# Optimization experiments

Measured on AMD Instinct MI355X. Metric: run time of the kernel, lower is better.

## Reference

```python
import jax, jax.numpy as jnp
import numpy as np

N = 50000          # num graph nodes
E = 800000         # edges per direction
NGRAM, ODIM = 4, 32
DIMS = [128, 128, 64]
CLASSES = 128
MAXPE = 10
L2_EPS = 1e-12


def setup_inputs() -> dict:
    key = jax.random.key(0)
    ks = iter(jax.random.split(key, 40))
    d = {}
    d['x'] = jax.random.normal(next(ks), (N, DIMS[0]), jnp.float32)
    d['edge_index_in'] = jax.random.randint(next(ks), (2, E), 0, N, dtype=jnp.int64)
    d['edge_weight_in'] = jax.random.uniform(next(ks), (E,), jnp.float32)
    d['edge_index_out'] = jax.random.randint(next(ks), (2, E), 0, N, dtype=jnp.int64)
    d['edge_weight_out'] = jax.random.uniform(next(ks), (E,), jnp.float32)
    d['pe_table'] = jax.random.normal(next(ks), (MAXPE, ODIM), jnp.float32) * 0.05
    # per-layer DirectGCNLayer params (weights stored [in,out], i.e. torch W.T)
    for l in range(2):
        di, do = DIMS[l], DIMS[l + 1]
        s = 1.0 / np.sqrt(di)
        d[f'W_main_in_{l}'] = jax.random.normal(next(ks), (di, do), jnp.float32) * s
        d[f'W_main_out_{l}'] = jax.random.normal(next(ks), (di, do), jnp.float32) * s
        d[f'W_shared_{l}'] = jax.random.normal(next(ks), (di, do), jnp.float32) * s
        d[f'b_main_in_{l}'] = jnp.zeros((do,), jnp.float32)
        d[f'b_main_out_{l}'] = jnp.zeros((do,), jnp.float32)
        d[f'b_shared_in_{l}'] = jnp.zeros((do,), jnp.float32)
        d[f'b_shared_out_{l}'] = jnp.zeros((do,), jnp.float32)
        d[f'C_in_{l}'] = jnp.ones((N, 1), jnp.float32)
        d[f'C_out_{l}'] = jnp.ones((N, 1), jnp.float32)
    # residual projection for layer 1 (128 -> 64); layer 0 is identity
    d['res_W_1'] = jax.random.normal(next(ks), (DIMS[1], DIMS[2]), jnp.float32) * (1.0 / np.sqrt(DIMS[1]))
    d['res_b_1'] = jnp.zeros((DIMS[2],), jnp.float32)
    d['dec_W'] = jax.random.normal(next(ks), (DIMS[2], CLASSES), jnp.float32) * (1.0 / np.sqrt(DIMS[2]))
    d['dec_b'] = jnp.zeros((CLASSES,), jnp.float32)
    return d


def _prop(xW, ei, ew):
    # gather source, scale by edge weight, scatter-add to target (PyG aggr='add')
    return jax.ops.segment_sum(ew[:, None] * xW[ei[0]], ei[1], num_segments=N)


def _layer(h, ei_in, ew_in, ei_out, ew_out,
           Wmi, Wmo, Ws, bmi, bmo, bsi, bso, cin, cout):
    xs = h @ Ws  # shared transform, propagated over both edge sets
    ic = _prop(h @ Wmi, ei_in, ew_in) + bmi + _prop(xs, ei_in, ew_in) + bsi
    oc = _prop(h @ Wmo, ei_out, ew_out) + bmo + _prop(xs, ei_out, ew_out) + bso
    return cin * ic + cout * oc


def reference(x, edge_index_in, edge_weight_in, edge_index_out, edge_weight_out,
              pe_table,
              W_main_in_0, W_main_out_0, W_shared_0, b_main_in_0, b_main_out_0,
              b_shared_in_0, b_shared_out_0, C_in_0, C_out_0,
              W_main_in_1, W_main_out_1, W_shared_1, b_main_in_1, b_main_out_1,
              b_shared_in_1, b_shared_out_1, C_in_1, C_out_1,
              res_W_1, res_b_1, dec_W, dec_b):
    # positional encoding: add pe[:n_gram_len] to each n-gram slot
    h = (x.reshape(N, NGRAM, ODIM) + pe_table[:NGRAM][None]).reshape(N, NGRAM * ODIM)
    # layer 0 (identity residual); dropout p=0 / eval -> no-op
    h = jnp.tanh(_layer(h, edge_index_in, edge_weight_in, edge_index_out, edge_weight_out,
                        W_main_in_0, W_main_out_0, W_shared_0, b_main_in_0, b_main_out_0,
                        b_shared_in_0, b_shared_out_0, C_in_0, C_out_0) + h)
    # layer 1 (linear residual projection 128 -> 64)
    h = jnp.tanh(_layer(h, edge_index_in, edge_weight_in, edge_index_out, edge_weight_out,
                        W_main_in_1, W_main_out_1, W_shared_1, b_main_in_1, b_main_out_1,
                        b_shared_in_1, b_shared_out_1, C_in_1, C_out_1)
                 + h @ res_W_1 + res_b_1)
    logits = h @ dec_W + dec_b
    logp = jax.nn.log_softmax(logits, axis=-1)
    emb = h / (jnp.linalg.norm(h, axis=1, keepdims=True) + L2_EPS)
    return logp, emb
```

## Files before the change

### kernel.cpp

```cpp
#include <hip/hip_runtime.h>
#include <hip/hip_bf16.h>
#include <math.h>

typedef __hip_bfloat16  bf16;
typedef __hip_bfloat162 bf162;
typedef __attribute__((ext_vector_type(8))) short short8;
typedef __attribute__((ext_vector_type(4))) float floatx4;
typedef __attribute__((ext_vector_type(2))) float floatx2;

#define BSZ     128
#define NBMAX   512
#define PACHUNK 8192

__device__ inline float4 bf4_to_f4(uint2 v) {
  float2 lo = __bfloat1622float2(*(bf162*)&v.x);
  float2 hi = __bfloat1622float2(*(bf162*)&v.y);
  return make_float4(lo.x, lo.y, hi.x, hi.y);
}
__device__ inline uint2 f4_to_bf4(float4 v) {
  bf162 lo = __float22bfloat162_rn(make_float2(v.x, v.y));
  bf162 hi = __float22bfloat162_rn(make_float2(v.z, v.w));
  uint2 r;
  r.x = *(unsigned*)&lo;
  r.y = *(unsigned*)&hi;
  return r;
}
__device__ inline floatx2 bf2_to_f2(unsigned u) {
  floatx2 r;
  r.x = __uint_as_float(u << 16);
  r.y = __uint_as_float(u & 0xffff0000u);
  return r;
}

__global__ __launch_bounds__(256) void k_bhist(const int* __restrict__ eiIn, const int* __restrict__ eiOut,
                                               int E, int* __restrict__ bcnt, int NB) {
  __shared__ int h[NBMAX];
  const int t = threadIdx.x;
  const int set = blockIdx.y;
  const int* dst = (set ? eiOut : eiIn) + E;
  for (int i = t; i < NB; i += 256) h[i] = 0;
  __syncthreads();
  const int base = blockIdx.x * PACHUNK;
  const int m = min(PACHUNK, E - base);
  #pragma unroll 4
  for (int r = 0; r < PACHUNK / 256; ++r) {
    int i = r * 256 + t;
    if (i < m) atomicAdd(&h[dst[base + i] >> 7], 1);
  }
  __syncthreads();
  for (int i = t; i < NB; i += 256) {
    int c = h[i];
    if (c) atomicAdd(&bcnt[set * NBMAX + i], c);
  }
}

__global__ __launch_bounds__(64) void k_bscan(const int* __restrict__ bcnt,
                                              int* __restrict__ BO, int* __restrict__ bcur, int NB) {
  const int set = blockIdx.x;
  const int t = threadIdx.x;
  int carry = 0;
  for (int base = 0; base < NB; base += 64) {
    int idx = base + t;
    int v = (idx < NB) ? bcnt[set * NBMAX + idx] : 0;
    int incl = v;
    #pragma unroll
    for (int d = 1; d < 64; d <<= 1) {
      int u = __shfl_up(incl, d, 64);
      if (t >= d) incl += u;
    }
    if (idx < NB) {
      int e = carry + incl - v;
      BO[set * NBMAX + idx]   = e;
      bcur[set * NBMAX + idx] = e;
    }
    carry += __shfl(incl, 63, 64);
  }
}

__global__ __launch_bounds__(256) void k_partA(const int* __restrict__ eiIn, const float* __restrict__ ewIn,
                                               const int* __restrict__ eiOut, const float* __restrict__ ewOut,
                                               int E, int* __restrict__ bucketCur,
                                               int2* __restrict__ sI, int2* __restrict__ sO, int NB) {
  __shared__ int2 staged[PACHUNK];
  __shared__ int cnt[NBMAX];
  __shared__ int sb[NBMAX];
  const int t = threadIdx.x;
  const int set = blockIdx.y;
  const int*   ei = set ? eiOut : eiIn;
  const float* ew = set ? ewOut : ewIn;
  int2* stg  = set ? sO : sI;
  int*  bcur = bucketCur + set * NBMAX;
  const int base = blockIdx.x * PACHUNK;
  const int m = min(PACHUNK, E - base);
  for (int b = t; b < NB; b += 256) cnt[b] = 0;
  __syncthreads();
  #pragma unroll 4
  for (int r = 0; r < PACHUNK / 256; ++r) {
    int i = r * 256 + t;
    if (i < m) atomicAdd(&cnt[ei[E + base + i] >> 7], 1);
  }
  __syncthreads();
  if (t < 64) {
    int carry = 0;
    int nch = (NB + 63) >> 6;
    for (int c = 0; c < nch; ++c) {
      int idx = c * 64 + t;
      int v = (idx < NB) ? cnt[idx] : 0;
      int incl = v;
      #pragma unroll
      for (int d = 1; d < 64; d <<= 1) {
        int u = __shfl_up(incl, d, 64);
        if (t >= d) incl += u;
      }
      if (idx < NB) sb[idx] = carry + incl - v;
      carry += __shfl(incl, 63, 64);
    }
  }
  __syncthreads();
  for (int b = t; b < NB; b += 256) {
    int c = cnt[b];
    if (c > 0) cnt[b] = atomicAdd(&bcur[b], c) - sb[b];
  }
  __syncthreads();
  #pragma unroll 4
  for (int r = 0; r < PACHUNK / 256; ++r) {
    int i = r * 256 + t;
    if (i < m) {
      int src = ei[base + i];
      int dst = ei[E + base + i];
      float w = ew[base + i];
      int b = dst >> 7;
      int rank = atomicAdd(&sb[b], 1);
      staged[rank] = make_int2(src | ((dst & 127) << 16) | (b << 23), __float_as_int(w));
    }
  }
  __syncthreads();
  #pragma unroll 4
  for (int r = 0; r < PACHUNK / 256; ++r) {
    int j = r * 256 + t;
    if (j < m) {
      int2 p = staged[j];
      int b = ((unsigned)p.x) >> 23;
      stg[cnt[b] + j] = p;
    }
  }
}

__global__ __launch_bounds__(256) void k_partB(const int* __restrict__ BO, const int* __restrict__ bcur,
                                               const int2* __restrict__ sI, const int2* __restrict__ sO,
                                               int2* __restrict__ eI, int2* __restrict__ eO,
                                               int* __restrict__ offsI, int* __restrict__ offsO, int N) {
  __shared__ int cnt[BSZ];
  __shared__ int excl[BSZ];
  __shared__ int cur[BSZ];
  const int t = threadIdx.x;
  const int b = blockIdx.x;
  const int set = blockIdx.y;
  const int2* stg = set ? sO : sI;
  int2* out = set ? eO : eI;
  int*  offs = set ? offsO : offsI;
  const int nlo = b << 7;
  const int nodes = min(BSZ, N - nlo);
  const int lo = BO[set * NBMAX + b];
  const int hi = bcur[set * NBMAX + b];
  if (t < BSZ) cnt[t] = 0;
  __syncthreads();
  for (int i = lo + t; i < hi; i += 256) atomicAdd(&cnt[(stg[i].x >> 16) & 127], 1);
  __syncthreads();
  if (t < 64) {
    int v0 = cnt[t];
    int i0 = v0;
    #pragma unroll
    for (int d = 1; d < 64; d <<= 1) { int u = __shfl_up(i0, d, 64); if (t >= d) i0 += u; }
    int v1 = cnt[64 + t];
    int i1 = v1;
    #pragma unroll
    for (int d = 1; d < 64; d <<= 1) { int u = __shfl_up(i1, d, 64); if (t >= d) i1 += u; }
    int tot0 = __shfl(i0, 63, 64);
    excl[t]      = i0 - v0;
    excl[64 + t] = tot0 + i1 - v1;
  }
  __syncthreads();
  if (t < BSZ) cur[t] = lo + excl[t];
  if (t < nodes) offs[nlo + t] = lo + excl[t];
  if (b == gridDim.x - 1 && t == 0) offs[N] = hi;
  __syncthreads();
  for (int i = lo + t; i < hi; i += 256) {
    int2 p = stg[i];
    int dl = (p.x >> 16) & 127;
    int pos = atomicAdd(&cur[dl], 1);
    out[pos] = make_int2(p.x & 0xffff, p.y);
  }
}

__device__ inline void pack_one(const float* __restrict__ W, bf16* __restrict__ P,
                                int id, int NT, int DO) {
  int lane = id & 63;
  int tile = id >> 6;
  int nt = tile % NT, kt = tile / NT;
  int col  = nt * 16 + (lane & 15);
  int krow = kt * 32 + (lane >> 4) * 8;
  bf16* dst = P + (size_t)id * 8;
  #pragma unroll
  for (int j = 0; j < 8; ++j) dst[j] = __float2bfloat16(W[(size_t)(krow + j) * DO + col]);
}
__global__ void k_packall(const float* __restrict__ Wmi0, const float* __restrict__ Wmo0,
                          const float* __restrict__ Ws0,
                          const float* __restrict__ Wmi1, const float* __restrict__ Wmo1,
                          const float* __restrict__ Ws1,
                          const float* __restrict__ resW, const float* __restrict__ Wd,
                          const float* __restrict__ bmi0, const float* __restrict__ bsi0,
                          const float* __restrict__ bmo0, const float* __restrict__ bso0,
                          const float* __restrict__ bmi1, const float* __restrict__ bsi1,
                          const float* __restrict__ bmo1, const float* __restrict__ bso1,
                          bf16* __restrict__ P0, bf16* __restrict__ P1, bf16* __restrict__ Pd,
                          float* __restrict__ bi0, float* __restrict__ bo0,
                          float* __restrict__ bi1, float* __restrict__ bo1) {
  int id = blockIdx.x * blockDim.x + threadIdx.x;
  const int T0 = 8 * 8 * 64;
  const int T1 = 4 * 12 * 64;
  const int Td = 2 * 8 * 64;
  if (id < T0) {
    int lane = id & 63, tile = id >> 6;
    int nt = tile % 8, kt = tile / 8;
    int col  = nt * 16 + (lane & 15);
    int krow = kt * 32 + (lane >> 4) * 8;
    bf16* dst = P0 + (size_t)id * 8;
    #pragma unroll
    for (int j = 0; j < 8; ++j) {
      int r = krow + j;
      float v = (r < 128 ? Wmi0[r * 128 + col] : Wmo0[(r - 128) * 128 + col])
              + Ws0[(r & 127) * 128 + col];
      dst[j] = __float2bfloat16(v);
    }
  } else if (id < T0 + T1) {
    int id1 = id - T0;
    int lane = id1 & 63, tile = id1 >> 6;
    int nt = tile % 12, kt = tile / 12;
    int col  = nt * 16 + (lane & 15);
    int krow = kt * 32 + (lane >> 4) * 8;
    bf16* dst = P1 + (size_t)id1 * 8;
    #pragma unroll
    for (int j = 0; j < 8; ++j) {
      int kp = krow + j;
      int k = ((kp & 7) << 4) + (kp >> 3);
      float v;
      if (col < 64)       v = Wmi1[k * 64 + col]       + Ws1[k * 64 + col];
      else if (col < 128) v = Wmo1[k * 64 + col - 64]  + Ws1[k * 64 + col - 64];
      else                v = resW[k * 64 + col - 128];
      dst[j] = __float2bfloat16(v);
    }
  } else if (id < T0 + T1 + Td) {
    pack_one(Wd, Pd, id - T0 - T1, 8, 128);
  } else {
    int j = id - (T0 + T1 + Td);
    if (j < 128) { bi0[j] = bmi0[j] + bsi0[j]; bo0[j] = bmo0[j] + bso0[j]; }
    if (j < 64)  { bi1[j] = bmi1[j] + bsi1[j]; bo1[j] = bmo1[j] + bso1[j]; }
  }
}

__global__ void k_prep0(const float* __restrict__ x, const float* __restrict__ pe,
                        bf16* __restrict__ h0, int total) {
  int i = blockIdx.x * blockDim.x + threadIdx.x;
  if (i < total) h0[i] = __float2bfloat16(x[i] + pe[i & 127]);
}

__global__ __launch_bounds__(256) void k_agg0(const bf16* __restrict__ tb,
                                              const int* __restrict__ offsI, const int2* __restrict__ eI,
                                              const int* __restrict__ offsO, const int2* __restrict__ eO,
                                              const float* __restrict__ cin, const float* __restrict__ cou,
                                              bf16* __restrict__ aggC, int N) {
  int n = (blockIdx.x * blockDim.x + threadIdx.x) >> 6;
  int lane = threadIdx.x & 63;
  if (n >= N) return;
  const int dir = lane >> 5;
  const int sub = (lane >> 4) & 1;
  const int sl  = lane & 15;
  const int*   offs = dir ? offsO : offsI;
  const int2*  el   = dir ? eO : eI;
  const float* cc   = dir ? cou : cin;
  const char* base = (const char*)tb + sl * 16;
  floatx2 A0 = {0.f, 0.f}, A1 = {0.f, 0.f}, A2 = {0.f, 0.f}, A3 = {0.f, 0.f};
  const int s0 = offs[n], s1 = offs[n + 1];
  int i = s0 + sub;
  for (; i + 6 < s1; i += 8) {
    int2 eA = el[i], eB = el[i + 2], eC = el[i + 4], eD = el[i + 6];
    uint4 vA = *(const uint4*)(base + ((size_t)(unsigned)eA.x << 8));
    uint4 vB = *(const uint4*)(base + ((size_t)(unsigned)eB.x << 8));
    uint4 vC = *(const uint4*)(base + ((size_t)(unsigned)eC.x << 8));
    uint4 vD = *(const uint4*)(base + ((size_t)(unsigned)eD.x << 8));
    float fA = __int_as_float(eA.y), fB = __int_as_float(eB.y);
    float fC = __int_as_float(eC.y), fD = __int_as_float(eD.y);
    floatx2 wA = {fA, fA}, wB = {fB, fB}, wC = {fC, fC}, wD = {fD, fD};
    A0 += wA * bf2_to_f2(vA.x) + wB * bf2_to_f2(vB.x) + wC * bf2_to_f2(vC.x) + wD * bf2_to_f2(vD.x);
    A1 += wA * bf2_to_f2(vA.y) + wB * bf2_to_f2(vB.y) + wC * bf2_to_f2(vC.y) + wD * bf2_to_f2(vD.y);
    A2 += wA * bf2_to_f2(vA.z) + wB * bf2_to_f2(vB.z) + wC * bf2_to_f2(vC.z) + wD * bf2_to_f2(vD.z);
    A3 += wA * bf2_to_f2(vA.w) + wB * bf2_to_f2(vB.w) + wC * bf2_to_f2(vC.w) + wD * bf2_to_f2(vD.w);
  }
  for (; i < s1; i += 2) {
    int2 e = el[i];
    uint4 v = *(const uint4*)(base + ((size_t)(unsigned)e.x << 8));
    float f = __int_as_float(e.y);
    floatx2 w2 = {f, f};
    A0 += w2 * bf2_to_f2(v.x);
    A1 += w2 * bf2_to_f2(v.y);
    A2 += w2 * bf2_to_f2(v.z);
    A3 += w2 * bf2_to_f2(v.w);
  }
  float a0 = A0.x, a1 = A0.y, a2 = A1.x, a3 = A1.y;
  float a4 = A2.x, a5 = A2.y, a6 = A3.x, a7 = A3.y;
  a0 += __shfl_xor(a0, 16, 64); a1 += __shfl_xor(a1, 16, 64);
  a2 += __shfl_xor(a2, 16, 64); a3 += __shfl_xor(a3, 16, 64);
  a4 += __shfl_xor(a4, 16, 64); a5 += __shfl_xor(a5, 16, 64);
  a6 += __shfl_xor(a6, 16, 64); a7 += __shfl_xor(a7, 16, 64);
  if (sub == 0) {
    float c = cc[n];
    uint2 plo = f4_to_bf4(make_float4(c * a0, c * a1, c * a2, c * a3));
    uint2 phi = f4_to_bf4(make_float4(c * a4, c * a5, c * a6, c * a7));
    *(uint4*)(aggC + (size_t)n * 256 + dir * 128 + sl * 8) = make_uint4(plo.x, plo.y, phi.x, phi.y);
  }
}

__global__ __launch_bounds__(256) void k_mf01(const bf16* __restrict__ A,
                                              const bf16* __restrict__ Wp0,
                                              const bf16* __restrict__ Wp1,
                                              const float* __restrict__ bi, const float* __restrict__ bo,
                                              const float* __restrict__ cin, const float* __restrict__ cou,
                                              const bf16* __restrict__ h0,
                                              bf16* __restrict__ t1g, bf16* __restrict__ t1r, int N) {
  __shared__ bf16 hs[64][136];
  const int lane = threadIdx.x & 63;
  const int wid  = threadIdx.x >> 6;
  const int quad = lane >> 4, lc = lane & 15;
  const int bmw = blockIdx.x * 64 + wid * 16;
  const int rowc = min(bmw + lc, N - 1);
  const bf16* ap = A + (size_t)rowc * 256 + quad * 8;
  const short8* bp = (const short8*)Wp0 + lane;
  floatx4 acc[8] = {};
  #pragma unroll
  for (int kt = 0; kt < 8; ++kt) {
    short8 af = *(const short8*)(ap + kt * 32);
    #pragma unroll
    for (int nt = 0; nt < 8; ++nt) {
      short8 bfr = bp[(kt * 8 + nt) * 64];
      acc[nt] = __builtin_amdgcn_mfma_f32_16x16x32_bf16(af, bfr, acc[nt], 0, 0, 0);
    }
  }
  float bif[8], bof[8];
  #pragma unroll
  for (int nt = 0; nt < 8; ++nt) {
    bif[nt] = bi[nt * 16 + lc];
    bof[nt] = bo[nt * 16 + lc];
  }
  #pragma unroll
  for (int r = 0; r < 4; ++r) {
    int gmc = min(bmw + quad * 4 + r, N - 1);
    float ci = cin[gmc], co = cou[gmc];
    unsigned hp[4];
    #pragma unroll
    for (int np = 0; np < 4; ++np) {
      int n0 = 2 * np, n1 = 2 * np + 1;
      float v0 = acc[n0][r] + ci * bif[n0] + co * bof[n0]
               + __bfloat162float(h0[(size_t)gmc * 128 + n0 * 16 + lc]);
      float v1 = acc[n1][r] + ci * bif[n1] + co * bof[n1]
               + __bfloat162float(h0[(size_t)gmc * 128 + n1 * 16 + lc]);
      bf162 p = __float22bfloat162_rn(make_float2(tanhf(v0), tanhf(v1)));
      hp[np] = *(unsigned*)&p;
    }
    *(uint4*)(&hs[wid * 16 + quad * 4 + r][lc * 8]) = make_uint4(hp[0], hp[1], hp[2], hp[3]);
  }
  __syncthreads();
  const short8* bp1 = (const short8*)Wp1 + lane;
  floatx4 acc2[12] = {};
  #pragma unroll
  for (int kt = 0; kt < 4; ++kt) {
    short8 af = *(const short8*)(&hs[wid * 16 + lc][kt * 32 + quad * 8]);
    #pragma unroll
    for (int nt = 0; nt < 12; ++nt) {
      short8 bfr = bp1[(kt * 12 + nt) * 64];
      acc2[nt] = __builtin_amdgcn_mfma_f32_16x16x32_bf16(af, bfr, acc2[nt], 0, 0, 0);
    }
  }
  #pragma unroll
  for (int r = 0; r < 4; ++r) {
    int gm = bmw + quad * 4 + r;
    if (gm < N) {
      #pragma unroll
      for (int nt = 0; nt < 12; ++nt) {
        int col = nt * 16 + lc;
        bf16 v = __float2bfloat16(acc2[nt][r]);
        if (col < 128) t1g[(size_t)gm * 128 + col]        = v;
        else           t1r[(size_t)gm * 64 + (col - 128)] = v;
      }
    }
  }
}

__global__ __launch_bounds__(256) void k_agg1(const bf16* __restrict__ t1g, const bf16* __restrict__ t1r,
                                              const int* __restrict__ offsI, const int2* __restrict__ eI,
                                              const int* __restrict__ offsO, const int2* __restrict__ eO,
                                              const float* __restrict__ bi, const float* __restrict__ bo,
                                              const float* __restrict__ resb,
                                              const float* __restrict__ cin, const float* __restrict__ cou,
                                              bf16* __restrict__ h2b, float* __restrict__ emb, int N) {
  int n = (blockIdx.x * blockDim.x + threadIdx.x) >> 6;
  int lane = threadIdx.x & 63;
  if (n >= N) return;
  const int dir = lane >> 5;
  const int sub = (lane >> 3) & 3;
  const int sl  = lane & 7;
  const int*   offs = dir ? offsO : offsI;
  const int2*  el   = dir ? eO : eI;
  const char* base = (const char*)t1g + dir * 128 + sl * 16;
  floatx2 A0 = {0.f, 0.f}, A1 = {0.f, 0.f}, A2 = {0.f, 0.f}, A3 = {0.f, 0.f};
  const int s0 = offs[n], s1 = offs[n + 1];
  int i = s0 + sub;
  for (; i + 12 < s1; i += 16) {
    int2 eA = el[i], eB = el[i + 4], eC = el[i + 8], eD = el[i + 12];
    uint4 vA = *(const uint4*)(base + ((size_t)(unsigned)eA.x << 8));
    uint4 vB = *(const uint4*)(base + ((size_t)(unsigned)eB.x << 8));
    uint4 vC = *(const uint4*)(base + ((size_t)(unsigned)eC.x << 8));
    uint4 vD = *(const uint4*)(base + ((size_t)(unsigned)eD.x << 8));
    float fA = __int_as_float(eA.y), fB = __int_as_float(eB.y);
    float fC = __int_as_float(eC.y), fD = __int_as_float(eD.y);
    floatx2 wA = {fA, fA}, wB = {fB, fB}, wC = {fC, fC}, wD = {fD, fD};
    A0 += wA * bf2_to_f2(vA.x) + wB * bf2_to_f2(vB.x) + wC * bf2_to_f2(vC.x) + wD * bf2_to_f2(vD.x);
    A1 += wA * bf2_to_f2(vA.y) + wB * bf2_to_f2(vB.y) + wC * bf2_to_f2(vC.y) + wD * bf2_to_f2(vD.y);
    A2 += wA * bf2_to_f2(vA.z) + wB * bf2_to_f2(vB.z) + wC * bf2_to_f2(vC.z) + wD * bf2_to_f2(vD.z);
    A3 += wA * bf2_to_f2(vA.w) + wB * bf2_to_f2(vB.w) + wC * bf2_to_f2(vC.w) + wD * bf2_to_f2(vD.w);
  }
  for (; i < s1; i += 4) {
    int2 e = el[i];
    uint4 v = *(const uint4*)(base + ((size_t)(unsigned)e.x << 8));
    float f = __int_as_float(e.y);
    floatx2 w2 = {f, f};
    A0 += w2 * bf2_to_f2(v.x);
    A1 += w2 * bf2_to_f2(v.y);
    A2 += w2 * bf2_to_f2(v.z);
    A3 += w2 * bf2_to_f2(v.w);
  }
  float a0 = A0.x, a1 = A0.y, a2 = A1.x, a3 = A1.y;
  float a4 = A2.x, a5 = A2.y, a6 = A3.x, a7 = A3.y;
  a0 += __shfl_xor(a0, 8, 64);  a1 += __shfl_xor(a1, 8, 64);
  a2 += __shfl_xor(a2, 8, 64);  a3 += __shfl_xor(a3, 8, 64);
  a4 += __shfl_xor(a4, 8, 64);  a5 += __shfl_xor(a5, 8, 64);
  a6 += __shfl_xor(a6, 8, 64);  a7 += __shfl_xor(a7, 8, 64);
  a0 += __shfl_xor(a0, 16, 64); a1 += __shfl_xor(a1, 16, 64);
  a2 += __shfl_xor(a2, 16, 64); a3 += __shfl_xor(a3, 16, 64);
  a4 += __shfl_xor(a4, 16, 64); a5 += __shfl_xor(a5, 16, 64);
  a6 += __shfl_xor(a6, 16, 64); a7 += __shfl_xor(a7, 16, 64);
  float b0 = __shfl_xor(a0, 32, 64), b1 = __shfl_xor(a1, 32, 64);
  float b2 = __shfl_xor(a2, 32, 64), b3 = __shfl_xor(a3, 32, 64);
  float b4 = __shfl_xor(a4, 32, 64), b5 = __shfl_xor(a5, 32, 64);
  float b6 = __shfl_xor(a6, 32, 64), b7 = __shfl_xor(a7, 32, 64);
  if (sub == 0) {
    const int c = sl * 8;
    float ci = cin[n], co = cou[n];
    float s_in[8]  = { dir ? b0 : a0, dir ? b1 : a1, dir ? b2 : a2, dir ? b3 : a3,
                       dir ? b4 : a4, dir ? b5 : a5, dir ? b6 : a6, dir ? b7 : a7 };
    float s_ou[8]  = { dir ? a0 : b0, dir ? a1 : b1, dir ? a2 : b2, dir ? a3 : b3,
                       dir ? a4 : b4, dir ? a5 : b5, dir ? a6 : b6, dir ? a7 : b7 };
    float4 bif0 = *(const float4*)(bi + c),   bif1 = *(const float4*)(bi + c + 4);
    float4 bof0 = *(const float4*)(bo + c),   bof1 = *(const float4*)(bo + c + 4);
    float4 rbf0 = *(const float4*)(resb + c), rbf1 = *(const float4*)(resb + c + 4);
    uint4 rvu = *(const uint4*)((const char*)t1r + (size_t)n * 128 + sl * 16);
    float4 rv0 = bf4_to_f4(make_uint2(rvu.x, rvu.y));
    float4 rv1 = bf4_to_f4(make_uint2(rvu.z, rvu.w));
    float bif[8] = { bif0.x, bif0.y, bif0.z, bif0.w, bif1.x, bif1.y, bif1.z, bif1.w };
    float bof[8] = { bof0.x, bof0.y, bof0.z, bof0.w, bof1.x, bof1.y, bof1.z, bof1.w };
    float rbf[8] = { rbf0.x, rbf0.y, rbf0.z, rbf0.w, rbf1.x, rbf1.y, rbf1.z, rbf1.w };
    float rvf[8] = { rv0.x, rv0.y, rv0.z, rv0.w, rv1.x, rv1.y, rv1.z, rv1.w };
    float v[8];
    float q = 0.f;
    #pragma unroll
    for (int k = 0; k < 8; ++k) {
      v[k] = tanhf(ci * (s_in[k] + bif[k]) + co * (s_ou[k] + bof[k]) + rvf[k] + rbf[k]);
      q += v[k] * v[k];
    }
    q += __shfl_xor(q, 1, 64);
    q += __shfl_xor(q, 2, 64);
    q += __shfl_xor(q, 4, 64);
    if (dir == 0) {
      uint2 plo = f4_to_bf4(make_float4(v[0], v[1], v[2], v[3]));
      uint2 phi = f4_to_bf4(make_float4(v[4], v[5], v[6], v[7]));
      *(uint4*)(h2b + (size_t)n * 64 + c) = make_uint4(plo.x, plo.y, phi.x, phi.y);
    } else {
      float inv = 1.0f / (sqrtf(q) + 1e-12f);
      *(float4*)(emb + (size_t)n * 64 + c)     = make_float4(v[0] * inv, v[1] * inv, v[2] * inv, v[3] * inv);
      *(float4*)(emb + (size_t)n * 64 + c + 4) = make_float4(v[4] * inv, v[5] * inv, v[6] * inv, v[7] * inv);
    }
  }
}

__global__ __launch_bounds__(256) void k_mfd(const bf16* __restrict__ A,
                                             const bf16* __restrict__ Wp,
                                             const float* __restrict__ bd,
                                             float* __restrict__ logp, int N) {
  const int lane = threadIdx.x & 63;
  const int quad = lane >> 4, lc = lane & 15;
  const int bmw = blockIdx.x * 64 + (threadIdx.x >> 6) * 16;
  const int rowc = min(bmw + lc, N - 1);
  const bf16* ap = A + (size_t)rowc * 64 + quad * 8;
  const short8* bp = (const short8*)Wp + lane;
  floatx4 acc[8] = {};
  #pragma unroll
  for (int kt = 0; kt < 2; ++kt) {
    short8 af = *(const short8*)(ap + kt * 32);
    #pragma unroll
    for (int nt = 0; nt < 8; ++nt) {
      short8 bfr = bp[(kt * 8 + nt) * 64];
      acc[nt] = __builtin_amdgcn_mfma_f32_16x16x32_bf16(af, bfr, acc[nt], 0, 0, 0);
    }
  }
  float bdv[8];
  #pragma unroll
  for (int nt = 0; nt < 8; ++nt) bdv[nt] = bd[nt * 16 + lc];
  #pragma unroll
  for (int r = 0; r < 4; ++r) {
    int gm = bmw + quad * 4 + r;
    float v[8];
    #pragma unroll
    for (int nt = 0; nt < 8; ++nt) v[nt] = acc[nt][r] + bdv[nt];
    float m = v[0];
    #pragma unroll
    for (int nt = 1; nt < 8; ++nt) m = fmaxf(m, v[nt]);
    #pragma unroll
    for (int d = 1; d < 16; d <<= 1) m = fmaxf(m, __shfl_xor(m, d, 64));
    float s = 0.f;
    #pragma unroll
    for (int nt = 0; nt < 8; ++nt) s += __expf(v[nt] - m);
    #pragma unroll
    for (int d = 1; d < 16; d <<= 1) s += __shfl_xor(s, d, 64);
    float lse = m + __logf(s);
    if (gm < N) {
      #pragma unroll
      for (int nt = 0; nt < 8; ++nt) logp[(size_t)gm * 128 + nt * 16 + lc] = v[nt] - lse;
    }
  }
}

extern "C" void kernel_launch(void* const* d_in, const int* in_sizes, int n_in,
                              void* d_out, int out_size, void* d_ws, size_t ws_size,
                              hipStream_t stream) {
  const float* x     = (const float*)d_in[0];
  const int*   ei_in = (const int*)d_in[1];
  const float* ew_in = (const float*)d_in[2];
  const int*   ei_ou = (const int*)d_in[3];
  const float* ew_ou = (const float*)d_in[4];
  const float* pe    = (const float*)d_in[5];
  const float* Wmi0  = (const float*)d_in[6];
  const float* Wmo0  = (const float*)d_in[7];
  const float* Wsh0  = (const float*)d_in[8];
  const float* bmi0  = (const float*)d_in[9];
  const float* bmo0  = (const float*)d_in[10];
  const float* bsi0  = (const float*)d_in[11];
  const float* bso0  = (const float*)d_in[12];
  const float* cin0  = (const float*)d_in[13];
  const float* cou0  = (const float*)d_in[14];
  const float* Wmi1  = (const float*)d_in[15];
  const float* Wmo1  = (const float*)d_in[16];
  const float* Wsh1  = (const float*)d_in[17];
  const float* bmi1  = (const float*)d_in[18];
  const float* bmo1  = (const float*)d_in[19];
  const float* bsi1  = (const float*)d_in[20];
  const float* bso1  = (const float*)d_in[21];
  const float* cin1  = (const float*)d_in[22];
  const float* cou1  = (const float*)d_in[23];
  const float* resW  = (const float*)d_in[24];
  const float* resb  = (const float*)d_in[25];
  const float* Wd    = (const float*)d_in[26];
  const float* bd    = (const float*)d_in[27];

  const int N = in_sizes[0] / 128;
  const int E = in_sizes[2];
  const int NB = (N + BSZ - 1) >> 7;

  char* ws = (char*)d_ws;
  size_t off = 0;
  auto alloc = [&](size_t bytes) -> char* {
    off = (off + 255) & ~(size_t)255;
    char* p = ws + off;
    off += bytes;
    return p;
  };
  bf16*  h0bf  = (bf16*)alloc((size_t)N * 128 * 2);
  bf16*  aggC  = (bf16*)alloc((size_t)N * 256 * 2);
  bf16*  h2b   = (bf16*)alloc((size_t)N * 64 * 2);
  bf16*  Wp0   = (bf16*)alloc(256 * 128 * 2);
  bf16*  Wp1   = (bf16*)alloc(128 * 192 * 2);
  bf16*  Wpd   = (bf16*)alloc(64 * 128 * 2);
  float* bi0   = (float*)alloc(128 * 4);
  float* bo0   = (float*)alloc(128 * 4);
  float* bi1   = (float*)alloc(64 * 4);
  float* bo1   = (float*)alloc(64 * 4);
  int*   bcnt  = (int*)alloc((size_t)2 * NBMAX * 4);
  int*   BO    = (int*)alloc((size_t)2 * NBMAX * 4);
  int*   bcur  = (int*)alloc((size_t)2 * NBMAX * 4);
  int*   offsI = (int*)alloc((size_t)(N + 1) * 4);
  int*   offsO = (int*)alloc((size_t)(N + 1) * 4);
  int2*  sI    = (int2*)alloc((size_t)E * 8);
  int2*  sO    = (int2*)alloc((size_t)E * 8);
  int2*  eI    = (int2*)alloc((size_t)E * 8);
  int2*  eO    = (int2*)alloc((size_t)E * 8);
  bf16* t1g = aggC;
  bf16* t1r = t1g + (size_t)N * 128;

  (void)hipMemsetAsync(bcnt, 0, (size_t)2 * NBMAX * 4, stream);

  dim3 gc((E + PACHUNK - 1) / PACHUNK, 2);
  k_bhist<<<gc, 256, 0, stream>>>(ei_in, ei_ou, E, bcnt, NB);
  k_bscan<<<2, 64, 0, stream>>>(bcnt, BO, bcur, NB);
  k_partA<<<gc, 256, 0, stream>>>(ei_in, ew_in, ei_ou, ew_ou, E, bcur, sI, sO, NB);
  dim3 gb(NB, 2);
  k_partB<<<gb, 256, 0, stream>>>(BO, bcur, sI, sO, eI, eO, offsI, offsO, N);
  k_packall<<<(8 * 8 * 64 + 4 * 12 * 64 + 2 * 8 * 64 + 128 + 255) / 256, 256, 0, stream>>>(
      Wmi0, Wmo0, Wsh0, Wmi1, Wmo1, Wsh1, resW, Wd,
      bmi0, bsi0, bmo0, bso0, bmi1, bsi1, bmo1, bso1,
      Wp0, Wp1, Wpd, bi0, bo0, bi1, bo1);
  k_prep0<<<(N * 128 + 255) / 256, 256, 0, stream>>>(x, pe, h0bf, N * 128);

  int ab = (N + 3) / 4;
  int mb = (N + 63) / 64;
  k_agg0<<<ab, 256, 0, stream>>>(h0bf, offsI, eI, offsO, eO, cin0, cou0, aggC, N);
  k_mf01<<<mb, 256, 0, stream>>>(aggC, Wp0, Wp1, bi0, bo0, cin0, cou0, h0bf, t1g, t1r, N);

  float* logp = (float*)d_out;
  float* emb  = logp + (size_t)N * 128;
  k_agg1<<<ab, 256, 0, stream>>>(t1g, t1r, offsI, eI, offsO, eO, bi1, bo1, resb, cin1, cou1,
                                 h2b, emb, N);
  k_mfd<<<mb, 256, 0, stream>>>(h2b, Wpd, bd, logp, N);
}
```

Baseline: 350.3 us.

## Slice layer-0 features into per-XCD column slabs for L2-local gathers

The bf16 input features are stored as four 32-column slabs, one per slice, instead of row-major. The layer-0 aggregation grid is remapped so that each slice is handled by blocks on a fixed pair of XCDs. The intent is that each XCD's L2 only caches a quarter of the feature table during the random gather. The kernel now launches 4x more blocks, and each one gathers 64-byte row fragments with 4 edges in flight per lane group. The residual read in k_mf01 is updated to the sliced layout, and the partition chunk size is halved.

```diff
diff --git a/kernel.cpp b/kernel.cpp
--- a/kernel.cpp
+++ b/kernel.cpp
@@ -10,7 +10,7 @@
 
 #define BSZ     128
 #define NBMAX   512
-#define PACHUNK 8192
+#define PACHUNK 4096
 
 __device__ inline float4 bf4_to_f4(uint2 v) {
   float2 lo = __bfloat1622float2(*(bf162*)&v.x);
@@ -260,64 +260,70 @@
 }
 
 __global__ void k_prep0(const float* __restrict__ x, const float* __restrict__ pe,
-                        bf16* __restrict__ h0, int total) {
+                        bf16* __restrict__ h0s, int N) {
   int i = blockIdx.x * blockDim.x + threadIdx.x;
-  if (i < total) h0[i] = __float2bfloat16(x[i] + pe[i & 127]);
-}
-
-__global__ __launch_bounds__(256) void k_agg0(const bf16* __restrict__ tb,
+  if (i >= N * 128) return;
+  int c = i & 31;
+  int t = i >> 5;
+  int s = t / N;
+  int n = t - s * N;
+  int d = s * 32 + c;
+  h0s[i] = __float2bfloat16(x[(size_t)n * 128 + d] + pe[d]);
+}
+
+__global__ __launch_bounds__(256) void k_agg0(const bf16* __restrict__ tbS,
                                               const int* __restrict__ offsI, const int2* __restrict__ eI,
                                               const int* __restrict__ offsO, const int2* __restrict__ eO,
                                               const float* __restrict__ cin, const float* __restrict__ cou,
                                               bf16* __restrict__ aggC, int N) {
-  int n = (blockIdx.x * blockDim.x + threadIdx.x) >> 6;
-  int lane = threadIdx.x & 63;
+  const int b = blockIdx.x;
+  const int xcd = b & 7;
+  const int slice = xcd >> 1;
+  const int half = xcd & 1;
+  const int worker = (b >> 3) * 2 + half;
+  const int wid = threadIdx.x >> 6;
+  const int lane = threadIdx.x & 63;
+  const int n = worker * 4 + wid;
   if (n >= N) return;
   const int dir = lane >> 5;
-  const int sub = (lane >> 4) & 1;
-  const int sl  = lane & 15;
+  const int sub = (lane >> 3) & 3;
+  const int sl  = lane & 7;
   const int*   offs = dir ? offsO : offsI;
   const int2*  el   = dir ? eO : eI;
   const float* cc   = dir ? cou : cin;
-  const char* base = (const char*)tb + sl * 16;
-  floatx2 A0 = {0.f, 0.f}, A1 = {0.f, 0.f}, A2 = {0.f, 0.f}, A3 = {0.f, 0.f};
+  const char* base = (const char*)tbS + (size_t)slice * N * 64 + sl * 8;
+  floatx2 A0 = {0.f, 0.f}, A1 = {0.f, 0.f};
   const int s0 = offs[n], s1 = offs[n + 1];
   int i = s0 + sub;
-  for (; i + 6 < s1; i += 8) {
-    int2 eA = el[i], eB = el[i + 2], eC = el[i + 4], eD = el[i + 6];
-    uint4 vA = *(const uint4*)(base + ((size_t)(unsigned)eA.x << 8));
-    uint4 vB = *(const uint4*)(base + ((size_t)(unsigned)eB.x << 8));
-    uint4 vC = *(const uint4*)(base + ((size_t)(unsigned)eC.x << 8));
-    uint4 vD = *(const uint4*)(base + ((size_t)(unsigned)eD.x << 8));
+  for (; i + 12 < s1; i += 16) {
+    int2 eA = el[i], eB = el[i + 4], eC = el[i + 8], eD = el[i + 12];
+    uint2 vA = *(const uint2*)(base + ((size_t)(unsigned)eA.x << 6));
+    uint2 vB = *(const uint2*)(base + ((size_t)(unsigned)eB.x << 6));
+    uint2 vC = *(const uint2*)(base + ((size_t)(unsigned)eC.x << 6));
+    uint2 vD = *(const uint2*)(base + ((size_t)(unsigned)eD.x << 6));
     float fA = __int_as_float(eA.y), fB = __int_as_float(eB.y);
     float fC = __int_as_float(eC.y), fD = __int_as_float(eD.y);
     floatx2 wA = {fA, fA}, wB = {fB, fB}, wC = {fC, fC}, wD = {fD, fD};
     A0 += wA * bf2_to_f2(vA.x) + wB * bf2_to_f2(vB.x) + wC * bf2_to_f2(vC.x) + wD * bf2_to_f2(vD.x);
     A1 += wA * bf2_to_f2(vA.y) + wB * bf2_to_f2(vB.y) + wC * bf2_to_f2(vC.y) + wD * bf2_to_f2(vD.y);
-    A2 += wA * bf2_to_f2(vA.z) + wB * bf2_to_f2(vB.z) + wC * bf2_to_f2(vC.z) + wD * bf2_to_f2(vD.z);
-    A3 += wA * bf2_to_f2(vA.w) + wB * bf2_to_f2(vB.w) + wC * bf2_to_f2(vC.w) + wD * bf2_to_f2(vD.w);
-  }
-  for (; i < s1; i += 2) {
+  }
+  for (; i < s1; i += 4) {
     int2 e = el[i];
-    uint4 v = *(const uint4*)(base + ((size_t)(unsigned)e.x << 8));
+    uint2 v = *(const uint2*)(base + ((size_t)(unsigned)e.x << 6));
     float f = __int_as_float(e.y);
     floatx2 w2 = {f, f};
     A0 += w2 * bf2_to_f2(v.x);
     A1 += w2 * bf2_to_f2(v.y);
-    A2 += w2 * bf2_to_f2(v.z);
-    A3 += w2 * bf2_to_f2(v.w);
   }
   float a0 = A0.x, a1 = A0.y, a2 = A1.x, a3 = A1.y;
-  float a4 = A2.x, a5 = A2.y, a6 = A3.x, a7 = A3.y;
+  a0 += __shfl_xor(a0, 8, 64);  a1 += __shfl_xor(a1, 8, 64);
+  a2 += __shfl_xor(a2, 8, 64);  a3 += __shfl_xor(a3, 8, 64);
   a0 += __shfl_xor(a0, 16, 64); a1 += __shfl_xor(a1, 16, 64);
   a2 += __shfl_xor(a2, 16, 64); a3 += __shfl_xor(a3, 16, 64);
-  a4 += __shfl_xor(a4, 16, 64); a5 += __shfl_xor(a5, 16, 64);
-  a6 += __shfl_xor(a6, 16, 64); a7 += __shfl_xor(a7, 16, 64);
   if (sub == 0) {
     float c = cc[n];
-    uint2 plo = f4_to_bf4(make_float4(c * a0, c * a1, c * a2, c * a3));
-    uint2 phi = f4_to_bf4(make_float4(c * a4, c * a5, c * a6, c * a7));
-    *(uint4*)(aggC + (size_t)n * 256 + dir * 128 + sl * 8) = make_uint4(plo.x, plo.y, phi.x, phi.y);
+    uint2 p = f4_to_bf4(make_float4(c * a0, c * a1, c * a2, c * a3));
+    *(uint2*)(aggC + (size_t)n * 256 + dir * 128 + slice * 32 + sl * 4) = p;
   }
 }
 
@@ -360,10 +366,11 @@
     #pragma unroll
     for (int np = 0; np < 4; ++np) {
       int n0 = 2 * np, n1 = 2 * np + 1;
+      const bf16* h0row = h0 + ((size_t)np * N + gmc) * 32;
       float v0 = acc[n0][r] + ci * bif[n0] + co * bof[n0]
-               + __bfloat162float(h0[(size_t)gmc * 128 + n0 * 16 + lc]);
+               + __bfloat162float(h0row[lc]);
       float v1 = acc[n1][r] + ci * bif[n1] + co * bof[n1]
-               + __bfloat162float(h0[(size_t)gmc * 128 + n1 * 16 + lc]);
+               + __bfloat162float(h0row[16 + lc]);
       bf162 p = __float22bfloat162_rn(make_float2(tanhf(v0), tanhf(v1)));
       hp[np] = *(unsigned*)&p;
     }
@@ -617,11 +624,13 @@
       Wmi0, Wmo0, Wsh0, Wmi1, Wmo1, Wsh1, resW, Wd,
       bmi0, bsi0, bmo0, bso0, bmi1, bsi1, bmo1, bso1,
       Wp0, Wp1, Wpd, bi0, bo0, bi1, bo1);
-  k_prep0<<<(N * 128 + 255) / 256, 256, 0, stream>>>(x, pe, h0bf, N * 128);
+  k_prep0<<<(N * 128 + 255) / 256, 256, 0, stream>>>(x, pe, h0bf, N);
 
   int ab = (N + 3) / 4;
   int mb = (N + 63) / 64;
-  k_agg0<<<ab, 256, 0, stream>>>(h0bf, offsI, eI, offsO, eO, cin0, cou0, aggC, N);
+  int nwork = (N + 3) / 4;
+  int gj = (nwork + 1) / 2;
+  k_agg0<<<gj * 8, 256, 0, stream>>>(h0bf, offsI, eI, offsO, eO, cin0, cou0, aggC, N);
   k_mf01<<<mb, 256, 0, stream>>>(aggC, Wp0, Wp1, bi0, bo0, cin0, cou0, h0bf, t1g, t1r, N);
 
   float* logp = (float*)d_out;
```

Result: slower. 391.7 us (+11.8%).
